# Optimization experiments

Measured on AMD Instinct MI355X. Metric: run time of the kernel, lower is better.

The kernel has to match this reference:

```python
import jax, jax.numpy as jnp
import numpy as np

B, N, L, D = 4, 128, 20, 512


def setup_inputs() -> dict:
    key = jax.random.key(0)
    ks = jax.random.split(key, 8)
    return {
        "f_b": jax.random.normal(ks[0], (B, N, D), jnp.float32),
        "f_w": jax.random.normal(ks[1], (B, L, D), jnp.float32),
        "f_s": jax.random.normal(ks[2], (B, D), jnp.float32),
        "f_m": jax.random.normal(ks[3], (B, N, N, D), jnp.float32),
        "Wq": jax.random.normal(ks[4], (D, D), jnp.float32) / np.sqrt(D).astype(np.float32),
        "bq": jax.random.normal(ks[5], (D,), jnp.float32) * 0.02,
        "Wk": jax.random.normal(ks[6], (D, D), jnp.float32) / np.sqrt(D).astype(np.float32),
        "bk": jax.random.normal(ks[7], (D,), jnp.float32) * 0.02,
    }


def reference(f_b, f_w, f_s, f_m, Wq, bq, Wk, bk):
    d = f_b.shape[-1]
    scale = jnp.asarray(1.0 / np.sqrt(d), f_b.dtype)
    # cross-attention: boundary features attend to word features
    q = f_b @ Wq.T + bq                                   # [B,N,D]
    k = f_w @ Wk.T + bk                                   # [B,L,D]
    attn = jax.nn.softmax(jnp.einsum('bnd,bld->bnl', q, k) * scale, axis=-1)
    f_baq = jnp.einsum('bnl,bld->bnd', attn, f_w)         # [B,N,D]
    # sentence-gated boundary features
    f_bq = f_b * (f_baq + f_s[:, None, :])                # [B,N,D]
    # boundary self-attention
    A_b = jax.nn.softmax(jnp.einsum('bnd,bmd->bnm', f_bq, f_bq) * scale, axis=-1)
    f_bb = jnp.einsum('bnm,bmd->bnd', A_b, f_b)           # [B,N,D]
    # gated moment-map reduction: sum_i A_b[b,i,j] * sigmoid(f_m*f_s)*f_m
    g_m = jax.nn.sigmoid(f_m * f_s[:, None, None, :])     # [B,N,N,D]
    f_bm = jnp.einsum('bij,bijd->bjd', A_b, g_m * f_m)    # [B,N,D]
    return f_bb + f_b + f_bm
```

## Files before the change

### kernel.cpp

```cpp
#include <hip/hip_runtime.h>
#include <hip/hip_bf16.h>

#define Bc 4
#define Nc 128
#define Lc 20
#define Dc 512
#define SCALE 0.04419417382415922f

#if __has_builtin(__builtin_amdgcn_exp2f)
#define EXP2(x) __builtin_amdgcn_exp2f(x)
#else
#define EXP2(x) __expf((x) * 0.6931471805599453f)
#endif

__global__ void fused_gemm(const float* __restrict__ f_b,
                           const float* __restrict__ f_w,
                           const float* __restrict__ Wq,
                           const float* __restrict__ bq,
                           const float* __restrict__ Wk,
                           const float* __restrict__ bk,
                           float* __restrict__ q,
                           float* __restrict__ k) {
    const bool is_q = blockIdx.y < 32;
    const float* A    = is_q ? f_b : f_w;
    const float* W    = is_q ? Wq : Wk;
    const float* bias = is_q ? bq : bk;
    float* C          = is_q ? q : k;
    const int row0 = (is_q ? blockIdx.y : (blockIdx.y - 32)) * 16;

    __shared__ float As[16][17];
    __shared__ float Ws[16][17];
    const int tx = threadIdx.x, ty = threadIdx.y;
    const int row  = row0 + ty;
    const int col0 = blockIdx.x * 16;
    const int col  = col0 + tx;
    float acc = 0.f;
    for (int k0 = 0; k0 < Dc; k0 += 16) {
        As[ty][tx] = A[row * Dc + k0 + tx];
        Ws[ty][tx] = W[(col0 + ty) * Dc + k0 + tx];
        __syncthreads();
#pragma unroll
        for (int kk = 0; kk < 16; kk++) acc += As[ty][kk] * Ws[tx][kk];
        __syncthreads();
    }
    C[row * Dc + col] = acc + bias[col];
}

__global__ void cross_attn_gate(const float* __restrict__ q,
                                const float* __restrict__ k,
                                const float* __restrict__ f_w,
                                const float* __restrict__ f_b,
                                const float* __restrict__ f_s,
                                float* __restrict__ f_bq) {
    const int bn = blockIdx.x;
    const int b  = bn >> 7;
    const int t  = threadIdx.x;
    const int lane = t & 63, wave = t >> 6;

    __shared__ float qs[Dc];
    __shared__ float sc[32];
    __shared__ float red0;

    qs[t]       = q[bn * Dc + t];
    qs[t + 256] = q[bn * Dc + t + 256];
    __syncthreads();

    for (int l = wave; l < Lc; l += 4) {
        const float* kr = k + (b * Lc + l) * Dc;
        float s = 0.f;
#pragma unroll
        for (int off = 0; off < Dc; off += 64) s += qs[lane + off] * kr[lane + off];
#pragma unroll
        for (int d = 32; d >= 1; d >>= 1) s += __shfl_down(s, d, 64);
        if (lane == 0) sc[l] = s * SCALE;
    }
    __syncthreads();

    if (t == 0) {
        float mx = sc[0];
        for (int l = 1; l < Lc; l++) mx = fmaxf(mx, sc[l]);
        float sum = 0.f;
        for (int l = 0; l < Lc; l++) { float e = __expf(sc[l] - mx); sc[l] = e; sum += e; }
        red0 = 1.0f / sum;
    }
    __syncthreads();
    const float inv = red0;

#pragma unroll
    for (int half = 0; half < 2; half++) {
        const int d = t + half * 256;
        float acc = 0.f;
#pragma unroll 4
        for (int l = 0; l < Lc; l++) acc += sc[l] * f_w[(b * Lc + l) * Dc + d];
        acc = acc * inv + f_s[b * Dc + d];
        f_bq[bn * Dc + d] = f_b[bn * Dc + d] * acc;
    }
}

__global__ void self_attn_scores(const float* __restrict__ f_bq,
                                 float* __restrict__ A_b,
                                 float* __restrict__ A_bT) {
    const int bn = blockIdx.x;
    const int b  = bn >> 7, n = bn & 127;
    const int t  = threadIdx.x;
    const int lane = t & 63, wave = t >> 6;

    __shared__ float qrow[Dc];
    __shared__ float sc[Nc];
    __shared__ float red[Nc];

    qrow[t]       = f_bq[bn * Dc + t];
    qrow[t + 256] = f_bq[bn * Dc + 256 + t];
    __syncthreads();

    const float4* q4 = (const float4*)qrow;
    const float4 qa = q4[lane];
    const float4 qb = q4[lane + 64];

    for (int m = wave; m < Nc; m += 4) {
        const float4* kr = (const float4*)(f_bq + (b * Nc + m) * Dc);
        const float4 va = kr[lane];
        const float4 vb = kr[lane + 64];
        float s = qa.x * va.x + qa.y * va.y + qa.z * va.z + qa.w * va.w
                + qb.x * vb.x + qb.y * vb.y + qb.z * vb.z + qb.w * vb.w;
#pragma unroll
        for (int d = 32; d >= 1; d >>= 1) s += __shfl_down(s, d, 64);
        if (lane == 0) sc[m] = s * SCALE;
    }
    __syncthreads();

    float e = 0.f, sval = 0.f;
    if (t < Nc) { sval = sc[t]; red[t] = sval; }
    __syncthreads();
    for (int st = 64; st >= 1; st >>= 1) {
        if (t < st) red[t] = fmaxf(red[t], red[t + st]);
        __syncthreads();
    }
    const float mx = red[0];
    __syncthreads();
    if (t < Nc) { e = __expf(sval - mx); red[t] = e; }
    __syncthreads();
    for (int st = 64; st >= 1; st >>= 1) {
        if (t < st) red[t] += red[t + st];
        __syncthreads();
    }
    if (t < Nc) {
        const float a = e * (1.0f / red[0]);
        A_b[bn * Nc + t] = a;
        A_bT[(b * Nc + t) * Nc + n] = a;
    }
}

__global__ void moment_final(const float* __restrict__ f_m,
                             const float* __restrict__ f_s,
                             const float* __restrict__ A_b,
                             const float* __restrict__ A_bT,
                             const float* __restrict__ f_b,
                             float* __restrict__ out) {
    const int bj = blockIdx.x;
    const int b  = bj >> 7, j = bj & 127;
    const int t  = threadIdx.x;
    const int c    = t & 127;
    const int half = t >> 7;

    __shared__ float w[Nc];
    __shared__ float ar[Nc];
    __shared__ float4 part[Nc];

    if (t < Nc) w[t] = A_bT[bj * Nc + t];
    else        ar[t - Nc] = A_b[bj * Nc + (t - Nc)];
    __syncthreads();

    const float4 s4 = ((const float4*)(f_s + b * Dc))[c];
    const float4 ns = make_float4(-1.4426950408889634f * s4.x,
                                  -1.4426950408889634f * s4.y,
                                  -1.4426950408889634f * s4.z,
                                  -1.4426950408889634f * s4.w);

    float4 acc = make_float4(0.f, 0.f, 0.f, 0.f);
    const float4* fm4 = (const float4*)f_m;
    int idx = ((b * Nc + half * 64) * Nc + j) * (Dc / 4) + c;

#pragma unroll 8
    for (int i = 0; i < 64; i++) {
        const float4 m4 = fm4[idx];
        idx += Nc * (Dc / 4);
        const float ww = w[half * 64 + i];
        acc.x += ww * m4.x * __builtin_amdgcn_rcpf(1.f + EXP2(m4.x * ns.x));
        acc.y += ww * m4.y * __builtin_amdgcn_rcpf(1.f + EXP2(m4.y * ns.y));
        acc.z += ww * m4.z * __builtin_amdgcn_rcpf(1.f + EXP2(m4.z * ns.z));
        acc.w += ww * m4.w * __builtin_amdgcn_rcpf(1.f + EXP2(m4.w * ns.w));
    }

    const float4* fb4 = (const float4*)(f_b + b * Nc * Dc);
#pragma unroll 4
    for (int m = half * 64; m < half * 64 + 64; m++) {
        const float a = ar[m];
        const float4 v = fb4[m * (Dc / 4) + c];
        acc.x += a * v.x; acc.y += a * v.y; acc.z += a * v.z; acc.w += a * v.w;
    }

    if (half == 1) part[c] = acc;
    __syncthreads();
    if (half == 0) {
        const float4 p = part[c];
        const float4 r = fb4[j * (Dc / 4) + c];
        acc.x += p.x + r.x; acc.y += p.y + r.y;
        acc.z += p.z + r.z; acc.w += p.w + r.w;
        ((float4*)out)[bj * (Dc / 4) + c] = acc;
    }
}

extern "C" void kernel_launch(void* const* d_in, const int* in_sizes, int n_in,
                              void* d_out, int out_size, void* d_ws, size_t ws_size,
                              hipStream_t stream) {
    const float* f_b = (const float*)d_in[0];
    const float* f_w = (const float*)d_in[1];
    const float* f_s = (const float*)d_in[2];
    const float* f_m = (const float*)d_in[3];
    const float* Wq  = (const float*)d_in[4];
    const float* bq  = (const float*)d_in[5];
    const float* Wk  = (const float*)d_in[6];
    const float* bk  = (const float*)d_in[7];
    float* out = (float*)d_out;

    float* ws   = (float*)d_ws;
    float* q    = ws;
    float* k    = q    + Bc*Nc*Dc;
    float* f_bq = k    + Bc*Lc*Dc;
    float* A_b  = f_bq + Bc*Nc*Dc;
    float* A_bT = A_b  + Bc*Nc*Nc;

    fused_gemm<<<dim3(Dc/16, 37), dim3(16,16), 0, stream>>>(f_b, f_w, Wq, bq, Wk, bk, q, k);
    cross_attn_gate<<<Bc*Nc, 256, 0, stream>>>(q, k, f_w, f_b, f_s, f_bq);
    self_attn_scores<<<Bc*Nc, 256, 0, stream>>>(f_bq, A_b, A_bT);
    moment_final<<<Bc*Nc, 256, 0, stream>>>(f_m, f_s, A_b, A_bT, f_b, out);
}
```

Before: 264.3 us.

## Split moment-map reduction over i into chunked partial kernel plus final reduce

The f_m gated reduction is split across four i-chunks in a separate kernel with 128-thread blocks (2048 blocks instead of 512), writing partial sums to workspace. A second kernel sums the partials and adds the A_b·f_b and residual terms. The aim is more blocks in flight, so the dominant f_m stream (128 MB) is read with more memory-level parallelism. The cost is an extra launch and an extra 4 MB write-and-read round trip for the partial sums.

```diff
diff --git a/kernel.cpp b/kernel.cpp
--- a/kernel.cpp
+++ b/kernel.cpp
@@ -151,11 +151,46 @@
     }
 }
 
-__global__ void moment_final(const float* __restrict__ f_m,
-                             const float* __restrict__ f_s,
+__global__ void moment_partial(const float* __restrict__ f_m,
+                               const float* __restrict__ f_s,
+                               const float* __restrict__ A_bT,
+                               float* __restrict__ part) {
+    const int bj    = blockIdx.x;
+    const int b     = bj >> 7, j = bj & 127;
+    const int chunk = blockIdx.y;
+    const int i0    = chunk * 32;
+    const int t     = threadIdx.x;
+
+    __shared__ float w[32];
+    if (t < 32) w[t] = A_bT[bj * Nc + i0 + t];
+    __syncthreads();
+
+    const float4 s4 = ((const float4*)(f_s + b * Dc))[t];
+    const float4 ns = make_float4(-1.4426950408889634f * s4.x,
+                                  -1.4426950408889634f * s4.y,
+                                  -1.4426950408889634f * s4.z,
+                                  -1.4426950408889634f * s4.w);
+
+    float4 acc = make_float4(0.f, 0.f, 0.f, 0.f);
+    const float4* fm4 = (const float4*)f_m;
+    int idx = ((b * Nc + i0) * Nc + j) * (Dc / 4) + t;
+
+#pragma unroll 8
+    for (int i = 0; i < 32; i++) {
+        const float4 m4 = fm4[idx];
+        idx += Nc * (Dc / 4);
+        const float ww = w[i];
+        acc.x += ww * m4.x * __builtin_amdgcn_rcpf(1.f + EXP2(m4.x * ns.x));
+        acc.y += ww * m4.y * __builtin_amdgcn_rcpf(1.f + EXP2(m4.y * ns.y));
+        acc.z += ww * m4.z * __builtin_amdgcn_rcpf(1.f + EXP2(m4.z * ns.z));
+        acc.w += ww * m4.w * __builtin_amdgcn_rcpf(1.f + EXP2(m4.w * ns.w));
+    }
+    ((float4*)part)[chunk * (Bc * Nc * Dc / 4) + bj * (Dc / 4) + t] = acc;
+}
+
+__global__ void final_reduce(const float* __restrict__ f_b,
                              const float* __restrict__ A_b,
-                             const float* __restrict__ A_bT,
-                             const float* __restrict__ f_b,
+                             const float* __restrict__ part,
                              float* __restrict__ out) {
     const int bj = blockIdx.x;
     const int b  = bj >> 7, j = bj & 127;
@@ -163,47 +198,32 @@
     const int c    = t & 127;
     const int half = t >> 7;
 
-    __shared__ float w[Nc];
-    __shared__ float ar[Nc];
-    __shared__ float4 part[Nc];
-
-    if (t < Nc) w[t] = A_bT[bj * Nc + t];
-    else        ar[t - Nc] = A_b[bj * Nc + (t - Nc)];
-    __syncthreads();
-
-    const float4 s4 = ((const float4*)(f_s + b * Dc))[c];
-    const float4 ns = make_float4(-1.4426950408889634f * s4.x,
-                                  -1.4426950408889634f * s4.y,
-                                  -1.4426950408889634f * s4.z,
-                                  -1.4426950408889634f * s4.w);
+    __shared__ float arow[Nc];
+    __shared__ float4 xch[Nc];
+
+    if (t < Nc) arow[t] = A_b[bj * Nc + t];
+    __syncthreads();
 
     float4 acc = make_float4(0.f, 0.f, 0.f, 0.f);
-    const float4* fm4 = (const float4*)f_m;
-    int idx = ((b * Nc + half * 64) * Nc + j) * (Dc / 4) + c;
-
+
+#pragma unroll
+    for (int cc = half * 2; cc < half * 2 + 2; cc++) {
+        const float4 p = ((const float4*)part)[cc * (Bc * Nc * Dc / 4) + bj * (Dc / 4) + c];
+        acc.x += p.x; acc.y += p.y; acc.z += p.z; acc.w += p.w;
+    }
+
+    const float4* fb4 = (const float4*)(f_b + b * Nc * Dc);
 #pragma unroll 8
-    for (int i = 0; i < 64; i++) {
-        const float4 m4 = fm4[idx];
-        idx += Nc * (Dc / 4);
-        const float ww = w[half * 64 + i];
-        acc.x += ww * m4.x * __builtin_amdgcn_rcpf(1.f + EXP2(m4.x * ns.x));
-        acc.y += ww * m4.y * __builtin_amdgcn_rcpf(1.f + EXP2(m4.y * ns.y));
-        acc.z += ww * m4.z * __builtin_amdgcn_rcpf(1.f + EXP2(m4.z * ns.z));
-        acc.w += ww * m4.w * __builtin_amdgcn_rcpf(1.f + EXP2(m4.w * ns.w));
-    }
-
-    const float4* fb4 = (const float4*)(f_b + b * Nc * Dc);
-#pragma unroll 4
     for (int m = half * 64; m < half * 64 + 64; m++) {
-        const float a = ar[m];
+        const float a = arow[m];
         const float4 v = fb4[m * (Dc / 4) + c];
         acc.x += a * v.x; acc.y += a * v.y; acc.z += a * v.z; acc.w += a * v.w;
     }
 
-    if (half == 1) part[c] = acc;
+    if (half == 1) xch[c] = acc;
     __syncthreads();
     if (half == 0) {
-        const float4 p = part[c];
+        const float4 p = xch[c];
         const float4 r = fb4[j * (Dc / 4) + c];
         acc.x += p.x + r.x; acc.y += p.y + r.y;
         acc.z += p.z + r.z; acc.w += p.w + r.w;
@@ -230,9 +250,11 @@
     float* f_bq = k    + Bc*Lc*Dc;
     float* A_b  = f_bq + Bc*Nc*Dc;
     float* A_bT = A_b  + Bc*Nc*Nc;
+    float* part = A_bT + Bc*Nc*Nc;
 
     fused_gemm<<<dim3(Dc/16, 37), dim3(16,16), 0, stream>>>(f_b, f_w, Wq, bq, Wk, bk, q, k);
     cross_attn_gate<<<Bc*Nc, 256, 0, stream>>>(q, k, f_w, f_b, f_s, f_bq);
     self_attn_scores<<<Bc*Nc, 256, 0, stream>>>(f_bq, A_b, A_bT);
-    moment_final<<<Bc*Nc, 256, 0, stream>>>(f_m, f_s, A_b, A_bT, f_b, out);
-}
+    moment_partial<<<dim3(Bc*Nc, 4), 128, 0, stream>>>(f_m, f_s, A_bT, part);
+    final_reduce<<<Bc*Nc, 256, 0, stream>>>(f_b, A_b, part, out);
+}
```

Result: slower. 270.3 us (+2.3%).

## Merge four kernels into one cooperative kernel with grid-wide syncs

Applied to the files above, without the earlier changes.

Replaces the four separate launches with one cooperative kernel of 512 blocks that runs the projection GEMM, cross-attention gate, self-attention scores and moment reduction as phases separated by grid.sync. The GEMM phase is retiled to 32x32 output tiles with a 2x2 register micro-tile, run by 304 blocks. This removes per-launch overhead and inter-kernel gaps, at the cost of grid barriers and a residency limit that requires all 512 blocks to be resident at once. The dominant f_m streaming phase is unchanged.

```diff
diff --git a/kernel.cpp b/kernel.cpp
--- a/kernel.cpp
+++ b/kernel.cpp
@@ -1,11 +1,14 @@
 #include <hip/hip_runtime.h>
-#include <hip/hip_bf16.h>
+#include <hip/hip_cooperative_groups.h>
+
+namespace cg = cooperative_groups;
 
 #define Bc 4
 #define Nc 128
 #define Lc 20
 #define Dc 512
 #define SCALE 0.04419417382415922f
+#define NL2E -1.4426950408889634f
 
 #if __has_builtin(__builtin_amdgcn_exp2f)
 #define EXP2(x) __builtin_amdgcn_exp2f(x)
@@ -13,201 +16,214 @@
 #define EXP2(x) __expf((x) * 0.6931471805599453f)
 #endif
 
-__global__ void fused_gemm(const float* __restrict__ f_b,
-                           const float* __restrict__ f_w,
-                           const float* __restrict__ Wq,
-                           const float* __restrict__ bq,
-                           const float* __restrict__ Wk,
-                           const float* __restrict__ bk,
-                           float* __restrict__ q,
-                           float* __restrict__ k) {
-    const bool is_q = blockIdx.y < 32;
-    const float* A    = is_q ? f_b : f_w;
-    const float* W    = is_q ? Wq : Wk;
-    const float* bias = is_q ? bq : bk;
-    float* C          = is_q ? q : k;
-    const int row0 = (is_q ? blockIdx.y : (blockIdx.y - 32)) * 16;
-
-    __shared__ float As[16][17];
-    __shared__ float Ws[16][17];
-    const int tx = threadIdx.x, ty = threadIdx.y;
-    const int row  = row0 + ty;
-    const int col0 = blockIdx.x * 16;
-    const int col  = col0 + tx;
-    float acc = 0.f;
-    for (int k0 = 0; k0 < Dc; k0 += 16) {
-        As[ty][tx] = A[row * Dc + k0 + tx];
-        Ws[ty][tx] = W[(col0 + ty) * Dc + k0 + tx];
-        __syncthreads();
-#pragma unroll
-        for (int kk = 0; kk < 16; kk++) acc += As[ty][kk] * Ws[tx][kk];
-        __syncthreads();
-    }
-    C[row * Dc + col] = acc + bias[col];
-}
-
-__global__ void cross_attn_gate(const float* __restrict__ q,
-                                const float* __restrict__ k,
-                                const float* __restrict__ f_w,
-                                const float* __restrict__ f_b,
-                                const float* __restrict__ f_s,
-                                float* __restrict__ f_bq) {
-    const int bn = blockIdx.x;
-    const int b  = bn >> 7;
-    const int t  = threadIdx.x;
+__global__ __launch_bounds__(256, 2)
+void mega(const float* __restrict__ f_b, const float* __restrict__ f_w,
+          const float* __restrict__ f_s, const float* __restrict__ f_m,
+          const float* __restrict__ Wq, const float* __restrict__ bq,
+          const float* __restrict__ Wk, const float* __restrict__ bk,
+          float* __restrict__ qb, float* __restrict__ kb,
+          float* __restrict__ f_bq, float* __restrict__ A_b,
+          float* __restrict__ A_bT, float* __restrict__ out)
+{
+    cg::grid_group grid = cg::this_grid();
+    const int blk  = blockIdx.x;
+    const int t    = threadIdx.x;
     const int lane = t & 63, wave = t >> 6;
 
-    __shared__ float qs[Dc];
-    __shared__ float sc[32];
-    __shared__ float red0;
-
-    qs[t]       = q[bn * Dc + t];
-    qs[t + 256] = q[bn * Dc + t + 256];
-    __syncthreads();
-
-    for (int l = wave; l < Lc; l += 4) {
-        const float* kr = k + (b * Lc + l) * Dc;
-        float s = 0.f;
-#pragma unroll
-        for (int off = 0; off < Dc; off += 64) s += qs[lane + off] * kr[lane + off];
-#pragma unroll
-        for (int d = 32; d >= 1; d >>= 1) s += __shfl_down(s, d, 64);
-        if (lane == 0) sc[l] = s * SCALE;
-    }
-    __syncthreads();
-
-    if (t == 0) {
-        float mx = sc[0];
-        for (int l = 1; l < Lc; l++) mx = fmaxf(mx, sc[l]);
-        float sum = 0.f;
-        for (int l = 0; l < Lc; l++) { float e = __expf(sc[l] - mx); sc[l] = e; sum += e; }
-        red0 = 1.0f / sum;
-    }
-    __syncthreads();
-    const float inv = red0;
-
-#pragma unroll
-    for (int half = 0; half < 2; half++) {
-        const int d = t + half * 256;
-        float acc = 0.f;
+    __shared__ __align__(16) float sm[1088];
+
+    if (blk < 304) {
+        const int tr = blk >> 4, tc = blk & 15;
+        const int c0 = tc * 32;
+        const bool isq = tr < 16;
+        const float* Ain  = isq ? f_b : f_w;
+        const float* W    = isq ? Wq : Wk;
+        const float* bias = isq ? bq : bk;
+        float* C          = isq ? qb : kb;
+        const int r0    = isq ? tr * 32 : (tr - 16) * 32;
+        const int nrows = isq ? 512 : 80;
+
+        float* As = sm;
+        float* Bs = sm + 544;
+
+        const int sr   = t >> 3;
+        const int sk2  = (t & 7) * 2;
+        const int arow = min(r0 + sr, nrows - 1);
+        const int wrow = c0 + sr;
+
+        const int ty2 = (t >> 4) * 2;
+        const int tx2 = (t & 15) * 2;
+        float a00 = 0.f, a01 = 0.f, a10 = 0.f, a11 = 0.f;
+
+        for (int k0 = 0; k0 < Dc; k0 += 16) {
+            const float2 ga = *(const float2*)&Ain[arow * Dc + k0 + sk2];
+            const float2 gb = *(const float2*)&W[wrow * Dc + k0 + sk2];
+            __syncthreads();
+            As[sk2 * 34 + sr]       = ga.x;
+            As[(sk2 + 1) * 34 + sr] = ga.y;
+            Bs[sk2 * 34 + sr]       = gb.x;
+            Bs[(sk2 + 1) * 34 + sr] = gb.y;
+            __syncthreads();
+#pragma unroll
+            for (int kk = 0; kk < 16; kk++) {
+                const float2 av = *(const float2*)&As[kk * 34 + ty2];
+                const float2 bv = *(const float2*)&Bs[kk * 34 + tx2];
+                a00 += av.x * bv.x; a01 += av.x * bv.y;
+                a10 += av.y * bv.x; a11 += av.y * bv.y;
+            }
+        }
+        const int orow = r0 + ty2;
+        const float b0 = bias[c0 + tx2], b1 = bias[c0 + tx2 + 1];
+        if (orow < nrows)
+            *(float2*)&C[orow * Dc + c0 + tx2] = make_float2(a00 + b0, a01 + b1);
+        if (orow + 1 < nrows)
+            *(float2*)&C[(orow + 1) * Dc + c0 + tx2] = make_float2(a10 + b0, a11 + b1);
+    }
+
+    __threadfence();
+    grid.sync();
+
+    {
+        const int bn = blk, b = bn >> 7;
+        float* qs = sm;
+        float* sc = sm + 512;
+
+        qs[t]       = qb[bn * Dc + t];
+        qs[t + 256] = qb[bn * Dc + t + 256];
+        __syncthreads();
+
+        for (int l = wave; l < Lc; l += 4) {
+            const float* kr = kb + (b * Lc + l) * Dc;
+            float s = 0.f;
+#pragma unroll
+            for (int off = 0; off < Dc; off += 64) s += qs[lane + off] * kr[lane + off];
+#pragma unroll
+            for (int d = 32; d >= 1; d >>= 1) s += __shfl_down(s, d, 64);
+            if (lane == 0) sc[l] = s * SCALE;
+        }
+        __syncthreads();
+
+        if (t == 0) {
+            float mx = sc[0];
+            for (int l = 1; l < Lc; l++) mx = fmaxf(mx, sc[l]);
+            float sum = 0.f;
+            for (int l = 0; l < Lc; l++) { float e = __expf(sc[l] - mx); sc[l] = e; sum += e; }
+            sm[544] = 1.0f / sum;
+        }
+        __syncthreads();
+        const float inv = sm[544];
+
+#pragma unroll
+        for (int half = 0; half < 2; half++) {
+            const int d = t + half * 256;
+            float acc = 0.f;
 #pragma unroll 4
-        for (int l = 0; l < Lc; l++) acc += sc[l] * f_w[(b * Lc + l) * Dc + d];
-        acc = acc * inv + f_s[b * Dc + d];
-        f_bq[bn * Dc + d] = f_b[bn * Dc + d] * acc;
-    }
-}
-
-__global__ void self_attn_scores(const float* __restrict__ f_bq,
-                                 float* __restrict__ A_b,
-                                 float* __restrict__ A_bT) {
-    const int bn = blockIdx.x;
-    const int b  = bn >> 7, n = bn & 127;
-    const int t  = threadIdx.x;
-    const int lane = t & 63, wave = t >> 6;
-
-    __shared__ float qrow[Dc];
-    __shared__ float sc[Nc];
-    __shared__ float red[Nc];
-
-    qrow[t]       = f_bq[bn * Dc + t];
-    qrow[t + 256] = f_bq[bn * Dc + 256 + t];
-    __syncthreads();
-
-    const float4* q4 = (const float4*)qrow;
-    const float4 qa = q4[lane];
-    const float4 qb = q4[lane + 64];
-
-    for (int m = wave; m < Nc; m += 4) {
-        const float4* kr = (const float4*)(f_bq + (b * Nc + m) * Dc);
-        const float4 va = kr[lane];
-        const float4 vb = kr[lane + 64];
-        float s = qa.x * va.x + qa.y * va.y + qa.z * va.z + qa.w * va.w
-                + qb.x * vb.x + qb.y * vb.y + qb.z * vb.z + qb.w * vb.w;
-#pragma unroll
-        for (int d = 32; d >= 1; d >>= 1) s += __shfl_down(s, d, 64);
-        if (lane == 0) sc[m] = s * SCALE;
-    }
-    __syncthreads();
-
-    float e = 0.f, sval = 0.f;
-    if (t < Nc) { sval = sc[t]; red[t] = sval; }
-    __syncthreads();
-    for (int st = 64; st >= 1; st >>= 1) {
-        if (t < st) red[t] = fmaxf(red[t], red[t + st]);
-        __syncthreads();
-    }
-    const float mx = red[0];
-    __syncthreads();
-    if (t < Nc) { e = __expf(sval - mx); red[t] = e; }
-    __syncthreads();
-    for (int st = 64; st >= 1; st >>= 1) {
-        if (t < st) red[t] += red[t + st];
-        __syncthreads();
-    }
-    if (t < Nc) {
-        const float a = e * (1.0f / red[0]);
-        A_b[bn * Nc + t] = a;
-        A_bT[(b * Nc + t) * Nc + n] = a;
-    }
-}
-
-__global__ void moment_final(const float* __restrict__ f_m,
-                             const float* __restrict__ f_s,
-                             const float* __restrict__ A_b,
-                             const float* __restrict__ A_bT,
-                             const float* __restrict__ f_b,
-                             float* __restrict__ out) {
-    const int bj = blockIdx.x;
-    const int b  = bj >> 7, j = bj & 127;
-    const int t  = threadIdx.x;
-    const int c    = t & 127;
-    const int half = t >> 7;
-
-    __shared__ float w[Nc];
-    __shared__ float ar[Nc];
-    __shared__ float4 part[Nc];
-
-    if (t < Nc) w[t] = A_bT[bj * Nc + t];
-    else        ar[t - Nc] = A_b[bj * Nc + (t - Nc)];
-    __syncthreads();
-
-    const float4 s4 = ((const float4*)(f_s + b * Dc))[c];
-    const float4 ns = make_float4(-1.4426950408889634f * s4.x,
-                                  -1.4426950408889634f * s4.y,
-                                  -1.4426950408889634f * s4.z,
-                                  -1.4426950408889634f * s4.w);
-
-    float4 acc = make_float4(0.f, 0.f, 0.f, 0.f);
-    const float4* fm4 = (const float4*)f_m;
-    int idx = ((b * Nc + half * 64) * Nc + j) * (Dc / 4) + c;
+            for (int l = 0; l < Lc; l++) acc += sc[l] * f_w[(b * Lc + l) * Dc + d];
+            acc = acc * inv + f_s[b * Dc + d];
+            f_bq[bn * Dc + d] = f_b[bn * Dc + d] * acc;
+        }
+    }
+
+    __threadfence();
+    grid.sync();
+
+    {
+        const int bn = blk, b = bn >> 7, n = bn & 127;
+        float* qrow = sm;
+        float* sc   = sm + 512;
+        float* red  = sm + 640;
+
+        qrow[t]       = f_bq[bn * Dc + t];
+        qrow[t + 256] = f_bq[bn * Dc + 256 + t];
+        __syncthreads();
+
+        const float4* q4 = (const float4*)qrow;
+        const float4 qa = q4[lane];
+        const float4 qv = q4[lane + 64];
+
+        for (int m = wave; m < Nc; m += 4) {
+            const float4* kr = (const float4*)(f_bq + (b * Nc + m) * Dc);
+            const float4 va = kr[lane];
+            const float4 vb = kr[lane + 64];
+            float s = qa.x * va.x + qa.y * va.y + qa.z * va.z + qa.w * va.w
+                    + qv.x * vb.x + qv.y * vb.y + qv.z * vb.z + qv.w * vb.w;
+#pragma unroll
+            for (int d = 32; d >= 1; d >>= 1) s += __shfl_down(s, d, 64);
+            if (lane == 0) sc[m] = s * SCALE;
+        }
+        __syncthreads();
+
+        float e = 0.f, sval = 0.f;
+        if (t < Nc) { sval = sc[t]; red[t] = sval; }
+        __syncthreads();
+        for (int st = 64; st >= 1; st >>= 1) {
+            if (t < st) red[t] = fmaxf(red[t], red[t + st]);
+            __syncthreads();
+        }
+        const float mx = red[0];
+        __syncthreads();
+        if (t < Nc) { e = __expf(sval - mx); red[t] = e; }
+        __syncthreads();
+        for (int st = 64; st >= 1; st >>= 1) {
+            if (t < st) red[t] += red[t + st];
+            __syncthreads();
+        }
+        if (t < Nc) {
+            const float a = e * (1.0f / red[0]);
+            A_b[bn * Nc + t] = a;
+            A_bT[(b * Nc + t) * Nc + n] = a;
+        }
+    }
+
+    __threadfence();
+    grid.sync();
+
+    {
+        const int bj = blk, b = bj >> 7, j = bj & 127;
+        const int c = t & 127, half = t >> 7;
+        float* w    = sm;
+        float* ar   = sm + 128;
+        float4* pex = (float4*)(sm + 256);
+
+        if (t < Nc) w[t] = A_bT[bj * Nc + t];
+        else        ar[t - Nc] = A_b[bj * Nc + (t - Nc)];
+        __syncthreads();
+
+        const float4 s4 = ((const float4*)(f_s + b * Dc))[c];
+        const float4 ns = make_float4(NL2E * s4.x, NL2E * s4.y, NL2E * s4.z, NL2E * s4.w);
+
+        float4 acc = make_float4(0.f, 0.f, 0.f, 0.f);
+        const float4* fm4 = (const float4*)f_m;
+        int idx = ((b * Nc + half * 64) * Nc + j) * (Dc / 4) + c;
 
 #pragma unroll 8
-    for (int i = 0; i < 64; i++) {
-        const float4 m4 = fm4[idx];
-        idx += Nc * (Dc / 4);
-        const float ww = w[half * 64 + i];
-        acc.x += ww * m4.x * __builtin_amdgcn_rcpf(1.f + EXP2(m4.x * ns.x));
-        acc.y += ww * m4.y * __builtin_amdgcn_rcpf(1.f + EXP2(m4.y * ns.y));
-        acc.z += ww * m4.z * __builtin_amdgcn_rcpf(1.f + EXP2(m4.z * ns.z));
-        acc.w += ww * m4.w * __builtin_amdgcn_rcpf(1.f + EXP2(m4.w * ns.w));
-    }
-
-    const float4* fb4 = (const float4*)(f_b + b * Nc * Dc);
+        for (int i = 0; i < 64; i++) {
+            const float4 m4 = fm4[idx];
+            idx += Nc * (Dc / 4);
+            const float ww = w[half * 64 + i];
+            acc.x += ww * m4.x * __builtin_amdgcn_rcpf(1.f + EXP2(m4.x * ns.x));
+            acc.y += ww * m4.y * __builtin_amdgcn_rcpf(1.f + EXP2(m4.y * ns.y));
+            acc.z += ww * m4.z * __builtin_amdgcn_rcpf(1.f + EXP2(m4.z * ns.z));
+            acc.w += ww * m4.w * __builtin_amdgcn_rcpf(1.f + EXP2(m4.w * ns.w));
+        }
+
+        const float4* fb4 = (const float4*)(f_b + b * Nc * Dc);
 #pragma unroll 4
-    for (int m = half * 64; m < half * 64 + 64; m++) {
-        const float a = ar[m];
-        const float4 v = fb4[m * (Dc / 4) + c];
-        acc.x += a * v.x; acc.y += a * v.y; acc.z += a * v.z; acc.w += a * v.w;
-    }
-
-    if (half == 1) part[c] = acc;
-    __syncthreads();
-    if (half == 0) {
-        const float4 p = part[c];
-        const float4 r = fb4[j * (Dc / 4) + c];
-        acc.x += p.x + r.x; acc.y += p.y + r.y;
-        acc.z += p.z + r.z; acc.w += p.w + r.w;
-        ((float4*)out)[bj * (Dc / 4) + c] = acc;
+        for (int m = half * 64; m < half * 64 + 64; m++) {
+            const float a = ar[m];
+            const float4 v = fb4[m * (Dc / 4) + c];
+            acc.x += a * v.x; acc.y += a * v.y; acc.z += a * v.z; acc.w += a * v.w;
+        }
+
+        if (half == 1) pex[c] = acc;
+        __syncthreads();
+        if (half == 0) {
+            const float4 p = pex[c];
+            const float4 r = fb4[j * (Dc / 4) + c];
+            acc.x += p.x + r.x; acc.y += p.y + r.y;
+            acc.z += p.z + r.z; acc.w += p.w + r.w;
+            ((float4*)out)[bj * (Dc / 4) + c] = acc;
+        }
     }
 }
 
@@ -222,17 +238,18 @@
     const float* bq  = (const float*)d_in[5];
     const float* Wk  = (const float*)d_in[6];
     const float* bk  = (const float*)d_in[7];
-    float* out = (float*)d_out;
+    float* outp = (float*)d_out;
 
     float* ws   = (float*)d_ws;
-    float* q    = ws;
-    float* k    = q    + Bc*Nc*Dc;
-    float* f_bq = k    + Bc*Lc*Dc;
-    float* A_b  = f_bq + Bc*Nc*Dc;
-    float* A_bT = A_b  + Bc*Nc*Nc;
-
-    fused_gemm<<<dim3(Dc/16, 37), dim3(16,16), 0, stream>>>(f_b, f_w, Wq, bq, Wk, bk, q, k);
-    cross_attn_gate<<<Bc*Nc, 256, 0, stream>>>(q, k, f_w, f_b, f_s, f_bq);
-    self_attn_scores<<<Bc*Nc, 256, 0, stream>>>(f_bq, A_b, A_bT);
-    moment_final<<<Bc*Nc, 256, 0, stream>>>(f_m, f_s, A_b, A_bT, f_b, out);
+    float* qb   = ws;
+    float* kb   = qb   + 512 * Dc;
+    float* f_bq = kb   + 80 * Dc;
+    float* A_b  = f_bq + 512 * Dc;
+    float* A_bT = A_b  + 512 * Nc;
+
+    void* args[] = {(void*)&f_b, (void*)&f_w, (void*)&f_s, (void*)&f_m,
+                    (void*)&Wq,  (void*)&bq,  (void*)&Wk,  (void*)&bk,
+                    (void*)&qb,  (void*)&kb,  (void*)&f_bq, (void*)&A_b,
+                    (void*)&A_bT, (void*)&outp};
+    hipLaunchCooperativeKernel((void*)mega, dim3(512), dim3(256), args, 0, stream);
 }
```

Measured after the change: 570.5 us. 2.16x slower.
